# Optimization experiments

Measured on AMD Instinct MI355X. Metric: run time of the kernel, lower is better.

## Reference

```python
import jax, jax.numpy as jnp
import numpy as np

RES = 32          # residual channels
SKIP = 32         # skip channels
Q2 = 3            # Volterra quadratic order
NUM_STACKS = 2
DILATIONS = [2 ** i for i in range(10)]  # dilations:int=9 -> [1,2,...,512]


def causal_conv(x, w, dilation=1):
    """Causal dilated conv1d. x: [B,C,T], w: [O,I,K] (torch layout)."""
    k = w.shape[-1]
    return jax.lax.conv_general_dilated(
        x, w, window_strides=(1,),
        padding=[(dilation * (k - 1), 0)],
        rhs_dilation=(dilation,),
        dimension_numbers=("NCH", "OIH", "NCH"))


def setup_inputs() -> dict:
    key = jax.random.key(0)
    ks = jax.random.split(key, 9)
    s = 0.05
    B, T = 8, 32000
    x = jax.random.normal(ks[0], (B, 1, T), dtype=jnp.float32)
    conv1_w = jax.random.normal(ks[1], (RES, 1, 3), dtype=jnp.float32) * s
    # one weight set per dilation level; shared across the 2 stacks
    res_w1 = jax.random.normal(ks[2], (len(DILATIONS), 2 * RES, RES, 3), dtype=jnp.float32) * s
    res_w2 = jax.random.normal(ks[3], (len(DILATIONS), RES + SKIP, RES, 1), dtype=jnp.float32) * s
    post2_w = jax.random.normal(ks[4], (16, SKIP, 3), dtype=jnp.float32) * s
    post3_w = jax.random.normal(ks[5], (8, 16, 3), dtype=jnp.float32) * s
    post4_w = jax.random.normal(ks[6], (1, 8, 3), dtype=jnp.float32) * s
    vnn1_w = jax.random.normal(ks[7], (1, 1, 16), dtype=jnp.float32) * s
    vnn2_w = jax.random.normal(ks[8], (2 * Q2 * 1, 1, 16), dtype=jnp.float32) * s
    return dict(x=x, conv1_w=conv1_w, res_w1=res_w1, res_w2=res_w2,
                post2_w=post2_w, post3_w=post3_w, post4_w=post4_w,
                vnn1_w=vnn1_w, vnn2_w=vnn2_w)


def reference(x, conv1_w, res_w1, res_w2, post2_w, post3_w, post4_w, vnn1_w, vnn2_w):
    h = causal_conv(x, conv1_w)                      # [B, RES, T]
    skip_sum = jnp.zeros_like(h[:, :SKIP, :])
    for _ in range(NUM_STACKS):
        for i, d in enumerate(DILATIONS):
            y = causal_conv(h, res_w1[i], dilation=d)       # [B, 2*RES, T]
            g = jnp.tanh(y[:, :RES]) * jax.nn.sigmoid(y[:, RES:2 * RES])
            z = causal_conv(g, res_w2[i])                   # [B, RES+SKIP, T] (1x1)
            h = h + z[:, :RES]
            skip_sum = skip_sum + z[:, RES:RES + SKIP]      # stack-then-sum == running sum
    out = jnp.tanh(skip_sum)
    out = jnp.tanh(causal_conv(out, post2_w))
    out = jnp.tanh(causal_conv(out, post3_w))
    out = jnp.tanh(causal_conv(out, post4_w))        # [B, 1, T]
    # VNN2 quadratic Volterra head
    lin = causal_conv(out, vnn1_w)                   # [B, 1, T]
    x2 = causal_conv(out, vnn2_w)                    # [B, 2*Q2, T]
    quad = jnp.sum(x2[:, :Q2] * x2[:, Q2:2 * Q2], axis=1, keepdims=True)
    return jnp.squeeze(lin + quad)                   # [B, T]
```

## Files before the change

kernel.cpp:

```cpp
#include <hip/hip_runtime.h>
#include <math.h>

#define T 32000
#define B 8
#define RES 32
#define SKIPC 32
#define NDIL 10
#define NLAYERS 20

typedef __attribute__((ext_vector_type(8))) _Float16 half8;
typedef __attribute__((ext_vector_type(4))) _Float16 half4;
typedef __attribute__((ext_vector_type(4))) float float4v;

__device__ __forceinline__ float fast_rcp(float x) { return __builtin_amdgcn_rcpf(x); }
__device__ __forceinline__ float fast_exp2(float x) { return __builtin_amdgcn_exp2f(x); }
__device__ __forceinline__ float fast_sigmoid(float x) {
    return fast_rcp(1.f + fast_exp2(-1.4426950408889634f * x));
}
__device__ __forceinline__ float fast_tanh(float x) {
    return 1.f - 2.f * fast_rcp(1.f + fast_exp2(2.8853900817779268f * x));
}

__device__ __forceinline__ void decode_bt(int g, int tile, int& b, int& t0) {
    b = g & 7;
    t0 = (g >> 3) * tile;
}

#define WROW 40
__device__ __forceinline__ void stage_w1(const _Float16* __restrict__ w1l,
                                         _Float16* w1s, int tid) {
    for (int i = tid; i < 192 * 4; i += 256) {
        int row = i >> 2, c = (i & 3) * 8;
        *(half8*)&w1s[row * WROW + c] = *(const half8*)(w1l + row * 32 + c);
    }
}
__device__ __forceinline__ void stage_w2(const _Float16* __restrict__ w2l,
                                         _Float16* w2s, int tid) {
    for (int i = tid; i < 64 * 4; i += 256) {
        int row = i >> 2, c = (i & 3) * 8;
        *(half8*)&w2s[row * WROW + c] = *(const half8*)(w2l + row * 32 + c);
    }
}

__global__ void repack_weights_f16(const float* __restrict__ w1,
                                   const float* __restrict__ w2,
                                   _Float16* __restrict__ w1f,
                                   _Float16* __restrict__ w2f) {
    int idx = blockIdx.x * blockDim.x + threadIdx.x;
    if (idx < NDIL * 3 * 64 * 32) {
        int i = idx;
        int c = i % 32; i /= 32;
        int o = i % 64; i /= 64;
        int kt = i % 3; i /= 3;
        int l = i;
        w1f[idx] = (_Float16)w1[((l * 64 + o) * 32 + c) * 3 + kt];
    }
    if (idx < NDIL * 64 * 32) {
        w2f[idx] = (_Float16)w2[idx];
    }
}

__global__ void conv1_kernel(const float* __restrict__ x,
                             const float* __restrict__ w,
                             _Float16* __restrict__ h) {
    int b, t0;
    decode_bt(blockIdx.x, 256, b, t0);
    int t = t0 + threadIdx.x;
    const float* xb = x + (size_t)b * T;
    float x2 = xb[t];
    float x1 = (t >= 1) ? xb[t - 1] : 0.f;
    float x0 = (t >= 2) ? xb[t - 2] : 0.f;
    _Float16* hr = h + ((size_t)b * T + t) * RES;
#pragma unroll
    for (int o = 0; o < RES; o += 8) {
        half8 v;
#pragma unroll
        for (int r = 0; r < 8; r++)
            v[r] = (_Float16)(w[(o + r) * 3 + 0] * x0 + w[(o + r) * 3 + 1] * x1
                            + w[(o + r) * 3 + 2] * x2);
        *(half8*)(hr + o) = v;
    }
}

template <bool FIRST>
__global__ __launch_bounds__(256) void res_layer_mfma(
        const _Float16* __restrict__ h_in, _Float16* __restrict__ h_out,
        _Float16* __restrict__ skip,
        const _Float16* __restrict__ w1l,
        const _Float16* __restrict__ w2l,
        int d) {
    __shared__ _Float16 Gs[4][32][40];
    __shared__ _Float16 w1s[192 * WROW];
    __shared__ _Float16 w2s[64 * WROW];

    const int tid = threadIdx.x;
    int b, t0;
    decode_bt(blockIdx.x, 128, b, t0);
    const int lane = tid & 63;
    const int wv = tid >> 6;
    const int n0 = wv * 32;
    const int lcol = lane & 15;
    const int q = lane >> 4;
    const _Float16* hb = h_in + (size_t)b * T * RES;

    stage_w1(w1l, w1s, tid);
    stage_w2(w2l, w2s, tid);

    half8 bf[2][3];
    const half8 zero8 = (half8)(_Float16)0.f;
    if (t0 >= 2 * d) {
#pragma unroll
        for (int nt = 0; nt < 2; nt++)
#pragma unroll
            for (int kt = 0; kt < 3; kt++) {
                int tb = t0 + n0 + nt * 16 + lcol - (2 - kt) * d;
                bf[nt][kt] = *(const half8*)(hb + (size_t)tb * RES + q * 8);
            }
    } else {
#pragma unroll
        for (int nt = 0; nt < 2; nt++)
#pragma unroll
            for (int kt = 0; kt < 3; kt++) {
                int tb = t0 + n0 + nt * 16 + lcol - (2 - kt) * d;
                bool ok = tb >= 0;
                half8 p = *(const half8*)(hb + (size_t)(ok ? tb : 0) * RES + q * 8);
                bf[nt][kt] = ok ? p : zero8;
            }
    }
    __syncthreads();

    float4v acc[4][2];
#pragma unroll
    for (int mt = 0; mt < 4; mt++)
#pragma unroll
        for (int nt = 0; nt < 2; nt++) acc[mt][nt] = (float4v)(0.f);
#pragma unroll
    for (int mt = 0; mt < 4; mt++)
#pragma unroll
        for (int kt = 0; kt < 3; kt++) {
            half8 af = *(const half8*)&w1s[(kt * 64 + mt * 16 + lcol) * WROW + q * 8];
#pragma unroll
            for (int nt = 0; nt < 2; nt++)
                acc[mt][nt] = __builtin_amdgcn_mfma_f32_16x16x32_f16(
                    af, bf[nt][kt], acc[mt][nt], 0, 0, 0);
        }

#pragma unroll
    for (int pp = 0; pp < 2; pp++)
#pragma unroll
        for (int nt = 0; nt < 2; nt++) {
            half4 gh;
#pragma unroll
            for (int r = 0; r < 4; r++)
                gh[r] = (_Float16)(fast_tanh(acc[pp][nt][r]) *
                                   fast_sigmoid(acc[pp + 2][nt][r]));
            *(half4*)&Gs[wv][nt * 16 + lcol][pp * 16 + q * 4] = gh;
        }
    __builtin_amdgcn_wave_barrier();

    const int tcol = t0 + n0;
    half4 skv[2][2];
    if (!FIRST) {
#pragma unroll
        for (int mt = 0; mt < 2; mt++)
#pragma unroll
            for (int nt = 0; nt < 2; nt++) {
                int t = tcol + nt * 16 + lcol;
                skv[mt][nt] = *(const half4*)(skip +
                    ((size_t)b * T + t) * SKIPC + mt * 16 + q * 4);
            }
    }

    float4v zacc[4][2];
#pragma unroll
    for (int mt = 0; mt < 4; mt++)
#pragma unroll
        for (int nt = 0; nt < 2; nt++) zacc[mt][nt] = (float4v)(0.f);
    half8 gb[2];
#pragma unroll
    for (int nt = 0; nt < 2; nt++)
        gb[nt] = *(const half8*)&Gs[wv][nt * 16 + lcol][q * 8];
#pragma unroll
    for (int mt = 0; mt < 4; mt++) {
        half8 af = *(const half8*)&w2s[(mt * 16 + lcol) * WROW + q * 8];
#pragma unroll
        for (int nt = 0; nt < 2; nt++)
            zacc[mt][nt] = __builtin_amdgcn_mfma_f32_16x16x32_f16(
                af, gb[nt], zacc[mt][nt], 0, 0, 0);
    }

#pragma unroll
    for (int mt = 0; mt < 2; mt++)
#pragma unroll
        for (int nt = 0; nt < 2; nt++) {
            int t = tcol + nt * 16 + lcol;
            size_t off = ((size_t)b * T + t) * RES + mt * 16 + q * 4;
            half4 hv = *(const half4*)(h_in + off);
            half4 hw;
#pragma unroll
            for (int r = 0; r < 4; r++)
                hw[r] = (_Float16)((float)hv[r] + zacc[mt][nt][r]);
            *(half4*)(h_out + off) = hw;
        }
#pragma unroll
    for (int mt = 0; mt < 2; mt++)
#pragma unroll
        for (int nt = 0; nt < 2; nt++) {
            int t = tcol + nt * 16 + lcol;
            size_t off = ((size_t)b * T + t) * SKIPC + mt * 16 + q * 4;
            half4 sw;
#pragma unroll
            for (int r = 0; r < 4; r++) {
                float z = zacc[mt + 2][nt][r];
                sw[r] = (_Float16)(FIRST ? z : (float)skv[mt][nt][r] + z);
            }
            *(half4*)(skip + off) = sw;
        }
}

template <bool FIRST>
__global__ __launch_bounds__(256) void res_pair_mfma(
        const _Float16* __restrict__ h_in, _Float16* __restrict__ h_out,
        _Float16* __restrict__ skip,
        const _Float16* __restrict__ w1A, const _Float16* __restrict__ w2A,
        const _Float16* __restrict__ w1B, const _Float16* __restrict__ w2B,
        int d1, int d2) {
    __shared__ _Float16 hAa[256][40];
    __shared__ _Float16 Gs[4][32][40];
    __shared__ _Float16 w1s[192 * WROW];
    __shared__ _Float16 w2s[64 * WROW];

    const int tid = threadIdx.x;
    int b, t0;
    decode_bt(blockIdx.x, 128, b, t0);
    const int lane = tid & 63;
    const int wv = tid >> 6;
    const int n0 = wv * 32;
    const int lcol = lane & 15;
    const int q = lane >> 4;
    const _Float16* hb = h_in + (size_t)b * T * RES;
    const half8 zero8 = (half8)(_Float16)0.f;

    float zAs[2][2][4];
    half4 hAcore[2][2];

    stage_w1(w1A, w1s, tid);
    stage_w2(w2A, w2s, tid);
    __syncthreads();

#pragma unroll 1
    for (int s = 0; s < 2; s++) {
        const int base = t0 - 128 + s * 128;

        half8 bf[2][3];
        if (base >= 2 * d1) {
#pragma unroll
            for (int nt = 0; nt < 2; nt++)
#pragma unroll
                for (int kt = 0; kt < 3; kt++) {
                    int tb = base + n0 + nt * 16 + lcol - (2 - kt) * d1;
                    bf[nt][kt] = *(const half8*)(hb + (size_t)tb * RES + q * 8);
                }
        } else {
#pragma unroll
            for (int nt = 0; nt < 2; nt++)
#pragma unroll
                for (int kt = 0; kt < 3; kt++) {
                    int tb = base + n0 + nt * 16 + lcol - (2 - kt) * d1;
                    bool ok = tb >= 0;
                    half8 p = *(const half8*)(hb + (size_t)(ok ? tb : 0) * RES + q * 8);
                    bf[nt][kt] = ok ? p : zero8;
                }
        }

        float4v acc[4][2];
#pragma unroll
        for (int mt = 0; mt < 4; mt++)
#pragma unroll
            for (int nt = 0; nt < 2; nt++) acc[mt][nt] = (float4v)(0.f);
#pragma unroll
        for (int mt = 0; mt < 4; mt++)
#pragma unroll
            for (int kt = 0; kt < 3; kt++) {
                half8 af = *(const half8*)&w1s[(kt * 64 + mt * 16 + lcol) * WROW + q * 8];
#pragma unroll
                for (int nt = 0; nt < 2; nt++)
                    acc[mt][nt] = __builtin_amdgcn_mfma_f32_16x16x32_f16(
                        af, bf[nt][kt], acc[mt][nt], 0, 0, 0);
            }

        __builtin_amdgcn_wave_barrier();
#pragma unroll
        for (int pp = 0; pp < 2; pp++)
#pragma unroll
            for (int nt = 0; nt < 2; nt++) {
                half4 gh;
#pragma unroll
                for (int r = 0; r < 4; r++)
                    gh[r] = (_Float16)(fast_tanh(acc[pp][nt][r]) *
                                       fast_sigmoid(acc[pp + 2][nt][r]));
                *(half4*)&Gs[wv][nt * 16 + lcol][pp * 16 + q * 4] = gh;
            }
        __builtin_amdgcn_wave_barrier();

        float4v zacc[4][2];
#pragma unroll
        for (int mt = 0; mt < 4; mt++)
#pragma unroll
            for (int nt = 0; nt < 2; nt++) zacc[mt][nt] = (float4v)(0.f);
        half8 gb[2];
#pragma unroll
        for (int nt = 0; nt < 2; nt++)
            gb[nt] = *(const half8*)&Gs[wv][nt * 16 + lcol][q * 8];
#pragma unroll
        for (int mt = 0; mt < 4; mt++) {
            half8 af = *(const half8*)&w2s[(mt * 16 + lcol) * WROW + q * 8];
#pragma unroll
            for (int nt = 0; nt < 2; nt++)
                zacc[mt][nt] = __builtin_amdgcn_mfma_f32_16x16x32_f16(
                    af, gb[nt], zacc[mt][nt], 0, 0, 0);
        }

#pragma unroll
        for (int mt = 0; mt < 2; mt++)
#pragma unroll
            for (int nt = 0; nt < 2; nt++) {
                int t = base + n0 + nt * 16 + lcol;
                bool ok = t >= 0;
                size_t off = ((size_t)b * T + (ok ? t : 0)) * RES + mt * 16 + q * 4;
                half4 hv = *(const half4*)(h_in + off);
                half4 hw;
#pragma unroll
                for (int r = 0; r < 4; r++)
                    hw[r] = ok ? (_Float16)((float)hv[r] + zacc[mt][nt][r])
                               : (_Float16)0.f;
                *(half4*)&hAa[s * 128 + n0 + nt * 16 + lcol][mt * 16 + q * 4] = hw;
                if (s == 1) {
                    hAcore[mt][nt] = hw;
#pragma unroll
                    for (int r = 0; r < 4; r++)
                        zAs[mt][nt][r] = zacc[mt + 2][nt][r];
                }
            }
    }
    __syncthreads();

    stage_w1(w1B, w1s, tid);
    stage_w2(w2B, w2s, tid);
    __syncthreads();

    half8 bf[2][3];
#pragma unroll
    for (int nt = 0; nt < 2; nt++)
#pragma unroll
        for (int kt = 0; kt < 3; kt++) {
            int rel = 128 + n0 + nt * 16 + lcol - (2 - kt) * d2;
            bf[nt][kt] = *(const half8*)&hAa[rel][q * 8];
        }

    float4v acc[4][2];
#pragma unroll
    for (int mt = 0; mt < 4; mt++)
#pragma unroll
        for (int nt = 0; nt < 2; nt++) acc[mt][nt] = (float4v)(0.f);
#pragma unroll
    for (int mt = 0; mt < 4; mt++)
#pragma unroll
        for (int kt = 0; kt < 3; kt++) {
            half8 af = *(const half8*)&w1s[(kt * 64 + mt * 16 + lcol) * WROW + q * 8];
#pragma unroll
            for (int nt = 0; nt < 2; nt++)
                acc[mt][nt] = __builtin_amdgcn_mfma_f32_16x16x32_f16(
                    af, bf[nt][kt], acc[mt][nt], 0, 0, 0);
        }

    __builtin_amdgcn_wave_barrier();
#pragma unroll
    for (int pp = 0; pp < 2; pp++)
#pragma unroll
        for (int nt = 0; nt < 2; nt++) {
            half4 gh;
#pragma unroll
            for (int r = 0; r < 4; r++)
                gh[r] = (_Float16)(fast_tanh(acc[pp][nt][r]) *
                                   fast_sigmoid(acc[pp + 2][nt][r]));
            *(half4*)&Gs[wv][nt * 16 + lcol][pp * 16 + q * 4] = gh;
        }
    __builtin_amdgcn_wave_barrier();

    const int tcol = t0 + n0;
    half4 skv[2][2];
    if (!FIRST) {
#pragma unroll
        for (int mt = 0; mt < 2; mt++)
#pragma unroll
            for (int nt = 0; nt < 2; nt++) {
                int t = tcol + nt * 16 + lcol;
                skv[mt][nt] = *(const half4*)(skip +
                    ((size_t)b * T + t) * SKIPC + mt * 16 + q * 4);
            }
    }

    float4v zacc[4][2];
#pragma unroll
    for (int mt = 0; mt < 4; mt++)
#pragma unroll
        for (int nt = 0; nt < 2; nt++) zacc[mt][nt] = (float4v)(0.f);
    half8 gb[2];
#pragma unroll
    for (int nt = 0; nt < 2; nt++)
        gb[nt] = *(const half8*)&Gs[wv][nt * 16 + lcol][q * 8];
#pragma unroll
    for (int mt = 0; mt < 4; mt++) {
        half8 af = *(const half8*)&w2s[(mt * 16 + lcol) * WROW + q * 8];
#pragma unroll
        for (int nt = 0; nt < 2; nt++)
            zacc[mt][nt] = __builtin_amdgcn_mfma_f32_16x16x32_f16(
                af, gb[nt], zacc[mt][nt], 0, 0, 0);
    }

#pragma unroll
    for (int mt = 0; mt < 2; mt++)
#pragma unroll
        for (int nt = 0; nt < 2; nt++) {
            int t = tcol + nt * 16 + lcol;
            size_t off = ((size_t)b * T + t) * RES + mt * 16 + q * 4;
            half4 hw;
#pragma unroll
            for (int r = 0; r < 4; r++)
                hw[r] = (_Float16)((float)hAcore[mt][nt][r] + zacc[mt][nt][r]);
            *(half4*)(h_out + off) = hw;
        }
#pragma unroll
    for (int mt = 0; mt < 2; mt++)
#pragma unroll
        for (int nt = 0; nt < 2; nt++) {
            int t = tcol + nt * 16 + lcol;
            size_t off = ((size_t)b * T + t) * SKIPC + mt * 16 + q * 4;
            half4 sw;
#pragma unroll
            for (int r = 0; r < 4; r++) {
                float z = zAs[mt][nt][r] + zacc[mt + 2][nt][r];
                sw[r] = (_Float16)(FIRST ? z : (float)skv[mt][nt][r] + z);
            }
            *(half4*)(skip + off) = sw;
        }
}

#define P2_TILE 256
__global__ __launch_bounds__(256) void post2_kernel(
        const _Float16* __restrict__ skip,
        const float* __restrict__ w,
        float* __restrict__ out16) {
    __shared__ float st[(P2_TILE + 2) * 33];

    const int tid = threadIdx.x;
    int b, t0;
    decode_bt(blockIdx.x, P2_TILE, b, t0);

    const int total8 = ((P2_TILE + 2) * 32) / 8;
    for (int ci = tid; ci < total8; ci += 256) {
        int flat = ci * 8;
        int row = flat >> 5;
        int c = flat & 31;
        int ts = t0 - 2 + row;
        half8 v = (half8)(_Float16)0.f;
        if (ts >= 0)
            v = *(const half8*)(skip + ((size_t)b * T + ts) * SKIPC + c);
        float* dst = &st[row * 33 + c];
#pragma unroll
        for (int r = 0; r < 8; r++)
            dst[r] = fast_tanh((float)v[r]);
    }
    __syncthreads();

    const int t = t0 + tid;
    float acc[16];
#pragma unroll
    for (int o = 0; o < 16; o++) acc[o] = 0.f;
#pragma unroll 4
    for (int c = 0; c < 32; c++) {
        float s0 = st[(tid + 0) * 33 + c];
        float s1 = st[(tid + 1) * 33 + c];
        float s2 = st[(tid + 2) * 33 + c];
#pragma unroll
        for (int o = 0; o < 16; o++) {
            const float* wo = w + (o * 32 + c) * 3;
            acc[o] += wo[0] * s0 + wo[1] * s1 + wo[2] * s2;
        }
    }
#pragma unroll
    for (int o = 0; o < 16; o++)
        out16[((size_t)(b * 16 + o)) * T + t] = fast_tanh(acc[o]);
}

__global__ void post3_kernel(const float* __restrict__ in16,
                             const float* __restrict__ w,
                             float* __restrict__ out8) {
    int b, t0;
    decode_bt(blockIdx.x, 256, b, t0);
    int t = t0 + threadIdx.x;
    float acc[8];
#pragma unroll
    for (int o = 0; o < 8; o++) acc[o] = 0.f;
    for (int c = 0; c < 16; c++) {
        const float* sc = in16 + ((size_t)(b * 16 + c)) * T;
        float v2 = sc[t];
        float v1 = (t >= 1) ? sc[t - 1] : 0.f;
        float v0 = (t >= 2) ? sc[t - 2] : 0.f;
#pragma unroll
        for (int o = 0; o < 8; o++) {
            const float* wo = w + (o * 16 + c) * 3;
            acc[o] += wo[0] * v0 + wo[1] * v1 + wo[2] * v2;
        }
    }
#pragma unroll
    for (int o = 0; o < 8; o++)
        out8[((size_t)(b * 8 + o)) * T + t] = fast_tanh(acc[o]);
}

__global__ __launch_bounds__(256) void post4_vnn_kernel(
        const float* __restrict__ in8,
        const float* __restrict__ w4,
        const float* __restrict__ w1,
        const float* __restrict__ w2,
        float* __restrict__ out) {
    __shared__ float s1[272];

    const int tid = threadIdx.x;
    int b, t0;
    decode_bt(blockIdx.x, 256, b, t0);

    for (int i = tid; i < 271; i += 256) {
        int c = t0 - 15 + i;
        float o1 = 0.f;
        if (c >= 0) {
            float acc = 0.f;
#pragma unroll
            for (int ch = 0; ch < 8; ch++) {
                const float* sc = in8 + ((size_t)(b * 8 + ch)) * T;
                float v2 = sc[c];
                float v1 = (c >= 1) ? sc[c - 1] : 0.f;
                float v0 = (c >= 2) ? sc[c - 2] : 0.f;
                const float* wo = w4 + ch * 3;
                acc += wo[0] * v0 + wo[1] * v1 + wo[2] * v2;
            }
            o1 = fast_tanh(acc);
        }
        s1[i] = o1;
    }
    __syncthreads();

    const int t = t0 + tid;
    float lin = 0.f;
    float s[6];
#pragma unroll
    for (int qq = 0; qq < 6; qq++) s[qq] = 0.f;
#pragma unroll
    for (int k = 0; k < 16; k++) {
        float tap = s1[tid + k];
        lin += w1[k] * tap;
#pragma unroll
        for (int qq = 0; qq < 6; qq++) s[qq] += w2[qq * 16 + k] * tap;
    }
    float quad = s[0] * s[3] + s[1] * s[4] + s[2] * s[5];
    out[(size_t)b * T + t] = lin + quad;
}

extern "C" void kernel_launch(void* const* d_in, const int* in_sizes, int n_in,
                              void* d_out, int out_size, void* d_ws, size_t ws_size,
                              hipStream_t stream) {
    const float* x       = (const float*)d_in[0];
    const float* conv1_w = (const float*)d_in[1];
    const float* res_w1  = (const float*)d_in[2];
    const float* res_w2  = (const float*)d_in[3];
    const float* post2_w = (const float*)d_in[4];
    const float* post3_w = (const float*)d_in[5];
    const float* post4_w = (const float*)d_in[6];
    const float* vnn1_w  = (const float*)d_in[7];
    const float* vnn2_w  = (const float*)d_in[8];
    float* out = (float*)d_out;

    char* ws = (char*)d_ws;
    const size_t SZ_HF   = (size_t)B * RES * T * 2;
    const size_t SZ_SKIP = (size_t)B * SKIPC * T * 2;
    const size_t SZ_O16  = (size_t)B * 16 * T * 4;
    const size_t SZ_O8   = (size_t)B * 8 * T * 4;
    _Float16*  hA    = (_Float16*)(ws);
    _Float16*  hB    = (_Float16*)(ws + SZ_HF);
    _Float16*  skip  = (_Float16*)(ws + 2 * SZ_HF);
    float*     out16 = (float*)(ws + 2 * SZ_HF + SZ_SKIP);
    float*     out8  = (float*)(ws + 2 * SZ_HF + SZ_SKIP + SZ_O16);
    _Float16*  w1f   = (_Float16*)(ws + 2 * SZ_HF + SZ_SKIP + SZ_O16 + SZ_O8);
    _Float16*  w2f   = (_Float16*)(ws + 2 * SZ_HF + SZ_SKIP + SZ_O16 + SZ_O8
                                      + (size_t)NDIL * 3 * 64 * 32 * 2);

    dim3 blk(256);
    dim3 grd(125 * 8);
    dim3 grdR(250 * 8);

    repack_weights_f16<<<dim3((NDIL * 3 * 64 * 32 + 255) / 256), blk, 0, stream>>>(
        res_w1, res_w2, w1f, w2f);

    conv1_kernel<<<grd, blk, 0, stream>>>(x, conv1_w, hA);

    const int  plan_l[13] = {0, 2, 4, 6, 7, 8, 9, 11, 13, 15, 17, 18, 19};
    const bool plan_p[13] = {true, true, true, false, false, false, true,
                             true, true, true, false, false, false};

    const _Float16* cur = hA;
    _Float16* nxt = hB;
    for (int i = 0; i < 13; i++) {
        int l = plan_l[i];
        int ilA = l % NDIL;
        int d1 = 1 << ilA;
        const _Float16* w1Ap = w1f + (size_t)ilA * 3 * 64 * 32;
        const _Float16* w2Ap = w2f + (size_t)ilA * 64 * 32;
        if (plan_p[i]) {
            int ilB = (l + 1) % NDIL;
            int d2 = 1 << ilB;
            const _Float16* w1Bp = w1f + (size_t)ilB * 3 * 64 * 32;
            const _Float16* w2Bp = w2f + (size_t)ilB * 64 * 32;
            if (i == 0)
                res_pair_mfma<true><<<grdR, blk, 0, stream>>>(
                    cur, nxt, skip, w1Ap, w2Ap, w1Bp, w2Bp, d1, d2);
            else
                res_pair_mfma<false><<<grdR, blk, 0, stream>>>(
                    cur, nxt, skip, w1Ap, w2Ap, w1Bp, w2Bp, d1, d2);
        } else {
            res_layer_mfma<false><<<grdR, blk, 0, stream>>>(
                cur, nxt, skip, w1Ap, w2Ap, d1);
        }
        const _Float16* tmp = nxt;
        nxt = (_Float16*)cur;
        cur = tmp;
    }

    post2_kernel<<<grd, blk, 0, stream>>>(skip, post2_w, out16);
    post3_kernel<<<grd, blk, 0, stream>>>(out16, post3_w, out8);
    post4_vnn_kernel<<<grd, blk, 0, stream>>>(out8, post4_w, vnn1_w, vnn2_w, out);
}
```

Baseline: 458.7 us.

## Fuse first five dilation layers into one halo-recompute kernel

Adds a res_f5 kernel that runs dilations 1..16 inside a single launch, with h tiles and a 64-sample causal halo held in double-buffered shared memory. Each layer recomputes the shrinking halo region, so the intermediate h tensors never go to global memory. The launch plan drops from 13 kernels to 10 residual kernels per pass. In exchange it does redundant MFMA work on the halo, restages weights every layer, and uses much more LDS, which may lower occupancy.

```diff
diff --git a/kernel.cpp b/kernel.cpp
--- a/kernel.cpp
+++ b/kernel.cpp
@@ -80,6 +80,187 @@
                             + w[(o + r) * 3 + 2] * x2);
         *(half8*)(hr + o) = v;
     }
+}
+
+template <bool FIRST>
+__global__ __launch_bounds__(256) void res_f5(
+        const _Float16* __restrict__ h_in, _Float16* __restrict__ h_out,
+        _Float16* __restrict__ skip,
+        const _Float16* __restrict__ w1f,
+        const _Float16* __restrict__ w2f) {
+    __shared__ _Float16 buf[2][192][40];
+    __shared__ _Float16 Gs[4][32][40];
+    __shared__ _Float16 w1s[192 * WROW];
+    __shared__ _Float16 w2s[64 * WROW];
+
+    const int tid = threadIdx.x;
+    int b, t0;
+    decode_bt(blockIdx.x, 128, b, t0);
+    const int lane = tid & 63;
+    const int wv = tid >> 6;
+    const int n0 = wv * 32;
+    const int lcol = lane & 15;
+    const int q = lane >> 4;
+    const half8 zero8 = (half8)(_Float16)0.f;
+
+    if (tid < 192) {
+        int col = t0 - 64 + tid;
+        bool ok = col >= 0;
+        const _Float16* src = h_in + ((size_t)b * T + (ok ? col : 0)) * RES;
+#pragma unroll
+        for (int c = 0; c < 4; c++) {
+            half8 v = ok ? *(const half8*)(src + c * 8) : zero8;
+            *(half8*)&buf[0][tid][c * 8] = v;
+        }
+    }
+
+    float ska[2][2][4];
+#pragma unroll
+    for (int mt = 0; mt < 2; mt++)
+#pragma unroll
+        for (int nt = 0; nt < 2; nt++)
+#pragma unroll
+            for (int r = 0; r < 4; r++) ska[mt][nt][r] = 0.f;
+
+    half4 hfin[2][2];
+
+    const int DIL[5]  = {1, 2, 4, 8, 16};
+    const int ROUT[5] = {60, 56, 48, 32, 0};
+
+    int cur = 0;
+#pragma unroll
+    for (int l = 0; l < 5; l++) {
+        __syncthreads();
+        stage_w1(w1f + (size_t)l * 3 * 64 * 32, w1s, tid);
+        stage_w2(w2f + (size_t)l * 64 * 32, w2s, tid);
+        __syncthreads();
+
+        const int d = DIL[l];
+        const int ro = ROUT[l];
+
+#pragma unroll
+        for (int s = 0; s < 2; s++) {
+            if (ro == 0 && s == 0) continue;
+
+            half8 bf_[2][3];
+#pragma unroll
+            for (int nt = 0; nt < 2; nt++) {
+                int u = n0 + nt * 16 + lcol;
+                int row = s ? (u + 64) : (u - 64);
+#pragma unroll
+                for (int kt = 0; kt < 3; kt++) {
+                    int tr = row - (2 - kt) * d;
+                    tr = tr < 0 ? 0 : tr;
+                    bf_[nt][kt] = *(const half8*)&buf[cur][tr][q * 8];
+                }
+            }
+
+            float4v acc[4][2];
+#pragma unroll
+            for (int mt = 0; mt < 4; mt++)
+#pragma unroll
+                for (int nt = 0; nt < 2; nt++) acc[mt][nt] = (float4v)(0.f);
+#pragma unroll
+            for (int mt = 0; mt < 4; mt++)
+#pragma unroll
+                for (int kt = 0; kt < 3; kt++) {
+                    half8 af = *(const half8*)&w1s[(kt * 64 + mt * 16 + lcol) * WROW + q * 8];
+#pragma unroll
+                    for (int nt = 0; nt < 2; nt++)
+                        acc[mt][nt] = __builtin_amdgcn_mfma_f32_16x16x32_f16(
+                            af, bf_[nt][kt], acc[mt][nt], 0, 0, 0);
+                }
+
+            __builtin_amdgcn_wave_barrier();
+#pragma unroll
+            for (int pp = 0; pp < 2; pp++)
+#pragma unroll
+                for (int nt = 0; nt < 2; nt++) {
+                    half4 gh;
+#pragma unroll
+                    for (int r = 0; r < 4; r++)
+                        gh[r] = (_Float16)(fast_tanh(acc[pp][nt][r]) *
+                                           fast_sigmoid(acc[pp + 2][nt][r]));
+                    *(half4*)&Gs[wv][nt * 16 + lcol][pp * 16 + q * 4] = gh;
+                }
+            __builtin_amdgcn_wave_barrier();
+
+            float4v zacc[4][2];
+#pragma unroll
+            for (int mt = 0; mt < 4; mt++)
+#pragma unroll
+                for (int nt = 0; nt < 2; nt++) zacc[mt][nt] = (float4v)(0.f);
+            half8 gb[2];
+#pragma unroll
+            for (int nt = 0; nt < 2; nt++)
+                gb[nt] = *(const half8*)&Gs[wv][nt * 16 + lcol][q * 8];
+#pragma unroll
+            for (int mt = 0; mt < 4; mt++) {
+                half8 af = *(const half8*)&w2s[(mt * 16 + lcol) * WROW + q * 8];
+#pragma unroll
+                for (int nt = 0; nt < 2; nt++)
+                    zacc[mt][nt] = __builtin_amdgcn_mfma_f32_16x16x32_f16(
+                        af, gb[nt], zacc[mt][nt], 0, 0, 0);
+            }
+
+#pragma unroll
+            for (int mt = 0; mt < 2; mt++)
+#pragma unroll
+                for (int nt = 0; nt < 2; nt++) {
+                    int u = n0 + nt * 16 + lcol;
+                    int row = s ? (u + 64) : (u - 64);
+                    bool live = s ? true : (u >= 128 - ro);
+                    int col = t0 - 128 + s * 128 + u;
+                    bool ok = col >= 0;
+                    int rr = row < 0 ? 0 : row;
+                    half4 hv = *(const half4*)&buf[cur][rr][mt * 16 + q * 4];
+                    half4 hw;
+#pragma unroll
+                    for (int r = 0; r < 4; r++)
+                        hw[r] = ok ? (_Float16)((float)hv[r] + zacc[mt][nt][r])
+                                   : (_Float16)0.f;
+                    if (l == 4) {
+                        hfin[mt][nt] = hw;
+                    } else if (live) {
+                        *(half4*)&buf[cur ^ 1][row][mt * 16 + q * 4] = hw;
+                    }
+                    if (s == 1) {
+#pragma unroll
+                        for (int r = 0; r < 4; r++)
+                            ska[mt][nt][r] += zacc[mt + 2][nt][r];
+                    }
+                }
+        }
+        cur ^= 1;
+    }
+
+    const int tcol = t0 + n0;
+    half4 skv[2][2];
+    if (!FIRST) {
+#pragma unroll
+        for (int mt = 0; mt < 2; mt++)
+#pragma unroll
+            for (int nt = 0; nt < 2; nt++) {
+                int t = tcol + nt * 16 + lcol;
+                skv[mt][nt] = *(const half4*)(skip +
+                    ((size_t)b * T + t) * SKIPC + mt * 16 + q * 4);
+            }
+    }
+#pragma unroll
+    for (int mt = 0; mt < 2; mt++)
+#pragma unroll
+        for (int nt = 0; nt < 2; nt++) {
+            int t = tcol + nt * 16 + lcol;
+            *(half4*)(h_out + ((size_t)b * T + t) * RES + mt * 16 + q * 4) =
+                hfin[mt][nt];
+            half4 sw;
+#pragma unroll
+            for (int r = 0; r < 4; r++) {
+                float z = ska[mt][nt][r];
+                sw[r] = (_Float16)(FIRST ? z : (float)skv[mt][nt][r] + z);
+            }
+            *(half4*)(skip + ((size_t)b * T + t) * SKIPC + mt * 16 + q * 4) = sw;
+        }
 }
 
 template <bool FIRST>
@@ -604,36 +785,38 @@
 
     conv1_kernel<<<grd, blk, 0, stream>>>(x, conv1_w, hA);
 
-    const int  plan_l[13] = {0, 2, 4, 6, 7, 8, 9, 11, 13, 15, 17, 18, 19};
-    const bool plan_p[13] = {true, true, true, false, false, false, true,
-                             true, true, true, false, false, false};
+    const size_t W1L = (size_t)3 * 64 * 32;
+    const size_t W2L = (size_t)64 * 32;
 
     const _Float16* cur = hA;
     _Float16* nxt = hB;
-    for (int i = 0; i < 13; i++) {
-        int l = plan_l[i];
-        int ilA = l % NDIL;
-        int d1 = 1 << ilA;
-        const _Float16* w1Ap = w1f + (size_t)ilA * 3 * 64 * 32;
-        const _Float16* w2Ap = w2f + (size_t)ilA * 64 * 32;
-        if (plan_p[i]) {
-            int ilB = (l + 1) % NDIL;
-            int d2 = 1 << ilB;
-            const _Float16* w1Bp = w1f + (size_t)ilB * 3 * 64 * 32;
-            const _Float16* w2Bp = w2f + (size_t)ilB * 64 * 32;
-            if (i == 0)
-                res_pair_mfma<true><<<grdR, blk, 0, stream>>>(
-                    cur, nxt, skip, w1Ap, w2Ap, w1Bp, w2Bp, d1, d2);
-            else
-                res_pair_mfma<false><<<grdR, blk, 0, stream>>>(
-                    cur, nxt, skip, w1Ap, w2Ap, w1Bp, w2Bp, d1, d2);
-        } else {
-            res_layer_mfma<false><<<grdR, blk, 0, stream>>>(
-                cur, nxt, skip, w1Ap, w2Ap, d1);
-        }
-        const _Float16* tmp = nxt;
-        nxt = (_Float16*)cur;
-        cur = tmp;
+
+    res_f5<true><<<grdR, blk, 0, stream>>>(cur, nxt, skip, w1f, w2f);
+    { const _Float16* tmp = nxt; nxt = (_Float16*)cur; cur = tmp; }
+
+    res_pair_mfma<false><<<grdR, blk, 0, stream>>>(
+        cur, nxt, skip, w1f + 5 * W1L, w2f + 5 * W2L,
+        w1f + 6 * W1L, w2f + 6 * W2L, 32, 64);
+    { const _Float16* tmp = nxt; nxt = (_Float16*)cur; cur = tmp; }
+
+    for (int il = 7; il <= 9; il++) {
+        res_layer_mfma<false><<<grdR, blk, 0, stream>>>(
+            cur, nxt, skip, w1f + (size_t)il * W1L, w2f + (size_t)il * W2L, 1 << il);
+        const _Float16* tmp = nxt; nxt = (_Float16*)cur; cur = tmp;
+    }
+
+    res_f5<false><<<grdR, blk, 0, stream>>>(cur, nxt, skip, w1f, w2f);
+    { const _Float16* tmp = nxt; nxt = (_Float16*)cur; cur = tmp; }
+
+    res_pair_mfma<false><<<grdR, blk, 0, stream>>>(
+        cur, nxt, skip, w1f + 5 * W1L, w2f + 5 * W2L,
+        w1f + 6 * W1L, w2f + 6 * W2L, 32, 64);
+    { const _Float16* tmp = nxt; nxt = (_Float16*)cur; cur = tmp; }
+
+    for (int il = 7; il <= 9; il++) {
+        res_layer_mfma<false><<<grdR, blk, 0, stream>>>(
+            cur, nxt, skip, w1f + (size_t)il * W1L, w2f + (size_t)il * W2L, 1 << il);
+        const _Float16* tmp = nxt; nxt = (_Float16*)cur; cur = tmp;
     }
 
     post2_kernel<<<grd, blk, 0, stream>>>(skip, post2_w, out16);
```

New measurement: 443.7 us. 3.3% less time.
